# Kernel tuning notes

Measured on AMD Instinct MI355X. Metric: run time of the kernel, lower is better.

Reference implementation:

```python
import jax, jax.numpy as jnp
import numpy as np
from jax import lax

N, G, E0, K = 16384, 128, 262144, 8   # nodes, graphs, initial edges, knn k
NF, D = 3, 8                          # num_features, smallest_dim


def _lin(key, fi, fo):
    k1, k2 = jax.random.split(key)
    lim = 1.0 / np.sqrt(fi)
    return (jax.random.uniform(k1, (fi, fo), minval=-lim, maxval=lim),
            jax.random.uniform(k2, (fo,), minval=-lim, maxval=lim))


def setup_inputs():
    key = jax.random.key(0)
    ks = jax.random.split(key, 16)
    x = jax.random.normal(ks[0], (N, NF), dtype=jnp.float32)
    edge_index = jax.random.randint(ks[1], (2, E0), 0, N, dtype=jnp.int32)
    batch = jnp.repeat(jnp.arange(G, dtype=jnp.int32), N // G)  # sorted graph ids
    p = {}
    dims = [("c1", 2 * NF, 2 * D, 2 * D), ("c2", 4 * D, D, D),
            ("c3", 2 * D, D, D), ("c4", 2 * D, 2 * D, 2 * D)]
    i = 2
    for name, fi, fh, fo in dims:
        p[name + "w1"], p[name + "b1"] = _lin(ks[i], fi, fh); i += 1
        p[name + "w2"], p[name + "b2"] = _lin(ks[i], fh, fo); i += 1
    p["fc3w"], p["fc3b"] = _lin(ks[i], 2 * D, 2 * NF); i += 1
    p["outw"], p["outb"] = _lin(ks[i], 2 * NF, 1)
    return {"x": x, "edge_index": edge_index, "batch": batch, **p}


def _edge_conv(x, src, dst, w1, b1, w2, b2):
    # PyG EdgeConv: message = MLP([x_i, x_j - x_i]), aggr='max' over incoming edges
    xi, xj = x[dst], x[src]
    m = jnp.concatenate([xi, xj - xi], axis=-1)        # [E, 2F]
    m = jax.nn.relu(m @ w1 + b1) @ w2 + b2             # [E, Fout]
    agg = jax.ops.segment_max(m, dst, num_segments=x.shape[0])
    return jnp.where(jnp.isfinite(agg), agg, 0.0)      # nodes w/o edges -> 0


def _knn_edges(x, k):
    # PyG knn_graph (no batch arg, loop=False, flow='source_to_target')
    n = x.shape[0]
    sq = jnp.sum(x * x, axis=1)
    d = sq[:, None] + sq[None, :] - 2.0 * (x @ x.T)    # [N, N] squared dists
    d = d.at[jnp.arange(n), jnp.arange(n)].set(jnp.inf)  # exclude self
    _, idx = lax.top_k(-d, k)                          # [N, k] nearest neighbors
    src = idx.reshape(-1).astype(jnp.int32)            # neighbor -> source
    dst = jnp.repeat(jnp.arange(n, dtype=jnp.int32), k)  # query -> target
    return src, dst


def reference(x, edge_index, batch,
              c1w1, c1b1, c1w2, c1b2, c2w1, c2b1, c2w2, c2b2,
              c3w1, c3b1, c3w2, c3b2, c4w1, c4b1, c4w2, c4b2,
              fc3w, fc3b, outw, outb):
    src0, dst0 = edge_index[0], edge_index[1]
    # encoder
    h = jax.nn.relu(_edge_conv(x, src0, dst0, c1w1, c1b1, c1w2, c1b2))
    h = jax.nn.relu(_edge_conv(h, src0, dst0, c2w1, c2b1, c2w2, c2b2))
    # dynamic graph rebuild
    src, dst = _knn_edges(h, K)
    # decoder (topk=False path: batch = data.batch)
    h = jax.nn.relu(_edge_conv(h, src, dst, c3w1, c3b1, c3w2, c3b2))
    h = jax.nn.relu(_edge_conv(h, src, dst, c4w1, c4b1, c4w2, c4b2))
    g = jax.ops.segment_max(h, batch, num_segments=G)  # global max pool [G, 2D]
    g = jnp.where(jnp.isfinite(g), g, 0.0)
    g = jax.nn.relu(g @ fc3w + fc3b)
    return jax.nn.sigmoid(g @ outw + outb)             # [G, 1]
```

## Files before the change

kernel.cpp:

```cpp
#include <hip/hip_runtime.h>
#include <math.h>

#define NN 16384
#define GG 128
#define KK 8
#define SCAP 96
#define TCAP 14
#define DCAP 64

__device__ __forceinline__ unsigned fkey(float x) {
  unsigned u = __float_as_uint(x);
  return (u & 0x80000000u) ? ~u : (u | 0x80000000u);
}

__device__ __forceinline__ float rdist2(const float* q, float4 c0, float4 c1,
                                        float sc) {
  float acc = fmaf(q[0], c0.x, sc);
  acc = fmaf(q[1], c0.y, acc);
  acc = fmaf(q[2], c0.z, acc);
  acc = fmaf(q[3], c0.w, acc);
  acc = fmaf(q[4], c1.x, acc);
  acc = fmaf(q[5], c1.y, acc);
  acc = fmaf(q[6], c1.z, acc);
  acc = fmaf(q[7], c1.w, acc);
  return acc;
}

__device__ __forceinline__ float4 neg2(float4 v) {
  return make_float4(-2.f * v.x, -2.f * v.y, -2.f * v.z, -2.f * v.w);
}

__global__ void k_build(const int* __restrict__ ei, int E,
                        int* __restrict__ deg, int* __restrict__ eidx) {
  int e = blockIdx.x * 256 + threadIdx.x;
  if (e >= E) return;
  int dv = ei[E + e];
  int slot = atomicAdd(&deg[dv], 1);
  if (slot < DCAP) eidx[dv * DCAP + slot] = e;
}

__global__ __launch_bounds__(256) void k_conv1g(
    const float* __restrict__ x, const int* __restrict__ ei,
    const int* __restrict__ deg, const int* __restrict__ eidx,
    const float* __restrict__ w1, const float* __restrict__ b1,
    const float* __restrict__ w2, const float* __restrict__ b2,
    float* __restrict__ h1out) {
  __shared__ float sw1[96], sb1[16], sw2[256], sb2[16];
  for (int t = threadIdx.x; t < 96; t += 256) sw1[t] = w1[t];
  for (int t = threadIdx.x; t < 256; t += 256) sw2[t] = w2[t];
  if (threadIdx.x < 16) {
    sb1[threadIdx.x] = b1[threadIdx.x];
    sb2[threadIdx.x] = b2[threadIdx.x];
  }
  __syncthreads();
  int tid = blockIdx.x * 256 + threadIdx.x;
  int i = tid >> 3, r = tid & 7;
  float xi0 = x[i * 3 + 0], xi1 = x[i * 3 + 1], xi2 = x[i * 3 + 2];
  float acc[16];
#pragma unroll
  for (int t = 0; t < 16; t++) acc[t] = -INFINITY;
  int n = deg[i];
  n = (n < DCAP) ? n : DCAP;
  for (int k = r; k < n; k += 8) {
    int e = eidx[i * DCAP + k];
    int s = ei[e];
    float m[6] = {xi0,
                  xi1,
                  xi2,
                  x[s * 3 + 0] - xi0,
                  x[s * 3 + 1] - xi1,
                  x[s * 3 + 2] - xi2};
    float hid[16];
#pragma unroll
    for (int o = 0; o < 16; o++) {
      float a = sb1[o];
#pragma unroll
      for (int f = 0; f < 6; f++) a = fmaf(m[f], sw1[f * 16 + o], a);
      hid[o] = fmaxf(a, 0.f);
    }
#pragma unroll
    for (int o = 0; o < 16; o++) {
      float a = sb2[o];
#pragma unroll
      for (int hh = 0; hh < 16; hh++) a = fmaf(hid[hh], sw2[hh * 16 + o], a);
      acc[o] = fmaxf(acc[o], a);
    }
  }
#pragma unroll
  for (int mm = 1; mm < 8; mm <<= 1) {
#pragma unroll
    for (int c = 0; c < 16; c++) acc[c] = fmaxf(acc[c], __shfl_xor(acc[c], mm));
  }
  if (r == 0) {
    float4* op = (float4*)(h1out + (size_t)i * 16);
    op[0] = make_float4(fmaxf(acc[0], 0.f), fmaxf(acc[1], 0.f),
                        fmaxf(acc[2], 0.f), fmaxf(acc[3], 0.f));
    op[1] = make_float4(fmaxf(acc[4], 0.f), fmaxf(acc[5], 0.f),
                        fmaxf(acc[6], 0.f), fmaxf(acc[7], 0.f));
    op[2] = make_float4(fmaxf(acc[8], 0.f), fmaxf(acc[9], 0.f),
                        fmaxf(acc[10], 0.f), fmaxf(acc[11], 0.f));
    op[3] = make_float4(fmaxf(acc[12], 0.f), fmaxf(acc[13], 0.f),
                        fmaxf(acc[14], 0.f), fmaxf(acc[15], 0.f));
  }
}

__global__ __launch_bounds__(256) void k_conv2g(
    const float* __restrict__ h1f, const int* __restrict__ ei,
    const int* __restrict__ deg, const int* __restrict__ eidx,
    const float* __restrict__ w1, const float* __restrict__ b1,
    const float* __restrict__ w2, const float* __restrict__ b2,
    float* __restrict__ h2out, float* __restrict__ sqn) {
  __shared__ float sw1[256], sb1[8], sw2[64], sb2[8];
  for (int t = threadIdx.x; t < 256; t += 256) sw1[t] = w1[t];
  if (threadIdx.x < 64) sw2[threadIdx.x] = w2[threadIdx.x];
  if (threadIdx.x < 8) {
    sb1[threadIdx.x] = b1[threadIdx.x];
    sb2[threadIdx.x] = b2[threadIdx.x];
  }
  __syncthreads();
  int tid = blockIdx.x * 256 + threadIdx.x;
  int i = tid >> 3, r = tid & 7;
  const float4* ip = (const float4*)(h1f + (size_t)i * 16);
  float4 a0 = ip[0], a1 = ip[1], a2 = ip[2], a3 = ip[3];
  float vi[16] = {a0.x, a0.y, a0.z, a0.w, a1.x, a1.y, a1.z, a1.w,
                  a2.x, a2.y, a2.z, a2.w, a3.x, a3.y, a3.z, a3.w};
  float acc[8];
#pragma unroll
  for (int t = 0; t < 8; t++) acc[t] = -INFINITY;
  int n = deg[i];
  n = (n < DCAP) ? n : DCAP;
  for (int k = r; k < n; k += 8) {
    int e = eidx[i * DCAP + k];
    int s = ei[e];
    const float4* jp = (const float4*)(h1f + (size_t)s * 16);
    float4 c0 = jp[0], c1 = jp[1], c2 = jp[2], c3 = jp[3];
    float vj[16] = {c0.x, c0.y, c0.z, c0.w, c1.x, c1.y, c1.z, c1.w,
                    c2.x, c2.y, c2.z, c2.w, c3.x, c3.y, c3.z, c3.w};
    float hid[8];
#pragma unroll
    for (int o = 0; o < 8; o++) {
      float a = sb1[o];
#pragma unroll
      for (int f = 0; f < 16; f++) a = fmaf(vi[f], sw1[f * 8 + o], a);
#pragma unroll
      for (int f = 0; f < 16; f++)
        a = fmaf(vj[f] - vi[f], sw1[(16 + f) * 8 + o], a);
      hid[o] = fmaxf(a, 0.f);
    }
#pragma unroll
    for (int o = 0; o < 8; o++) {
      float a = sb2[o];
#pragma unroll
      for (int hh = 0; hh < 8; hh++) a = fmaf(hid[hh], sw2[hh * 8 + o], a);
      acc[o] = fmaxf(acc[o], a);
    }
  }
#pragma unroll
  for (int mm = 1; mm < 8; mm <<= 1) {
#pragma unroll
    for (int c = 0; c < 8; c++) acc[c] = fmaxf(acc[c], __shfl_xor(acc[c], mm));
  }
  if (r == 0) {
    float v[8];
    float s2 = 0.f;
#pragma unroll
    for (int c = 0; c < 8; c++) {
      v[c] = fmaxf(acc[c], 0.f);
      s2 += v[c] * v[c];
    }
    float4* op = (float4*)(h2out + (size_t)i * 8);
    op[0] = make_float4(v[0], v[1], v[2], v[3]);
    op[1] = make_float4(v[4], v[5], v[6], v[7]);
    sqn[i] = s2;
  }
}

__global__ __launch_bounds__(256) void k_tau_part(
    const float* __restrict__ h2f, const float* __restrict__ sqn,
    float* __restrict__ taupart) {
  __shared__ float sh[512 * 8];
  __shared__ float ss[512];
  int qb = blockIdx.x & 63;
  int scn = blockIdx.x >> 6;
  int i = qb * 256 + threadIdx.x;
  const float4* qp = (const float4*)(h2f + (size_t)i * 8);
  float4 q0 = qp[0], q1 = qp[1];
  float q[8] = {q0.x, q0.y, q0.z, q0.w, q1.x, q1.y, q1.z, q1.w};
  int base = scn * 512;
  for (int cc = threadIdx.x; cc < 512; cc += 256) {
    const float4* src = (const float4*)(h2f + (size_t)(base + cc) * 8);
    ((float4*)sh)[cc * 2] = neg2(src[0]);
    ((float4*)sh)[cc * 2 + 1] = neg2(src[1]);
    ss[cc] = sqn[base + cc];
  }
  __syncthreads();
  float bd[8];
#pragma unroll
  for (int t = 0; t < 8; t++) bd[t] = INFINITY;
  int self = i - base;
#pragma unroll 2
  for (int c = 0; c < 512; c++) {
    const float4* cp = (const float4*)(sh + c * 8);
    float r = rdist2(q, cp[0], cp[1], ss[c]);
    float cd = (c == self) ? INFINITY : r;
#pragma unroll
    for (int t = 0; t < 8; t++) {
      float lo = fminf(cd, bd[t]);
      cd = fmaxf(cd, bd[t]);
      bd[t] = lo;
    }
  }
  float* dst = taupart + ((size_t)scn * NN + i) * 8;
#pragma unroll
  for (int t = 0; t < 8; t++) dst[t] = bd[t];
}

__global__ void k_tau_merge(const float* __restrict__ taupart,
                            float* __restrict__ tau) {
  int i = blockIdx.x * blockDim.x + threadIdx.x;
  if (i >= NN) return;
  float bd[8];
#pragma unroll
  for (int t = 0; t < 8; t++) bd[t] = INFINITY;
  for (int scn = 0; scn < 8; scn++) {
    const float* p = taupart + ((size_t)scn * NN + i) * 8;
#pragma unroll
    for (int c = 0; c < 8; c++) {
      float cd = p[c];
#pragma unroll
      for (int t = 0; t < 8; t++) {
        float lo = fminf(cd, bd[t]);
        cd = fmaxf(cd, bd[t]);
        bd[t] = lo;
      }
    }
  }
  tau[i] = bd[7];
}

__global__ __launch_bounds__(256, 4) void k_knn_collect(
    const float* __restrict__ h2f, const float* __restrict__ sqn,
    const float* __restrict__ tau, int* __restrict__ qcnt,
    unsigned long long* __restrict__ surv) {
  __shared__ float sh[256 * 8];
  __shared__ float ss[256];
  __shared__ unsigned long long pbuf[TCAP * 256];
  int qb = blockIdx.x & 15;
  int ch = blockIdx.x >> 4;
  float q[4][8];
  float thr[4];
#pragma unroll
  for (int s = 0; s < 4; s++) {
    int ii = qb * 1024 + threadIdx.x + s * 256;
    const float4* qp = (const float4*)(h2f + (size_t)ii * 8);
    float4 a = qp[0], b = qp[1];
    q[s][0] = a.x; q[s][1] = a.y; q[s][2] = a.z; q[s][3] = a.w;
    q[s][4] = b.x; q[s][5] = b.y; q[s][6] = b.z; q[s][7] = b.w;
    thr[s] = tau[ii];
  }
  int base = ch * 256;
  {
    const float4* src = (const float4*)(h2f + (size_t)(base + threadIdx.x) * 8);
    ((float4*)sh)[threadIdx.x * 2] = neg2(src[0]);
    ((float4*)sh)[threadIdx.x * 2 + 1] = neg2(src[1]);
    ss[threadIdx.x] = sqn[base + threadIdx.x];
  }
  __syncthreads();
  int cnt = 0;
#pragma unroll 2
  for (int c = 0; c < 256; c++) {
    const float4* cp = (const float4*)(sh + c * 8);
    float4 c0 = cp[0], c1 = cp[1];
    float sc = ss[c];
#pragma unroll
    for (int s = 0; s < 4; s++) {
      float r = rdist2(q[s], c0, c1, sc);
      if (__any(r <= thr[s])) {
        int j = base + c;
        int iqs = qb * 1024 + threadIdx.x + s * 256;
        if (r <= thr[s] && j != iqs) {
          if (cnt < TCAP)
            pbuf[cnt * 256 + threadIdx.x] =
                ((unsigned long long)fkey(r) << 32) | (unsigned)(s << 14) |
                (unsigned)j;
          cnt++;
        }
      }
    }
  }
  int n = (cnt < TCAP) ? cnt : TCAP;
  for (int k = 0; k < n; k++) {
    unsigned long long e = pbuf[k * 256 + threadIdx.x];
    int s = (int)((e >> 14) & 3u);
    unsigned long long key = e & 0xFFFFFFFF00003FFFull;
    int qi = qb * 1024 + threadIdx.x + s * 256;
    int slot = atomicAdd(&qcnt[qi], 1);
    if (slot < SCAP) surv[(size_t)qi * SCAP + slot] = key;
  }
}

__global__ __launch_bounds__(256) void k_mc3(
    const float* __restrict__ h2f, const int* __restrict__ qcnt,
    const unsigned long long* __restrict__ surv,
    const float* __restrict__ w1, const float* __restrict__ b1,
    const float* __restrict__ w2, const float* __restrict__ b2,
    int* __restrict__ kn, float* __restrict__ h3) {
  __shared__ float sw1[128], sb1[8], sw2[64], sb2[8];
  if (threadIdx.x < 128) sw1[threadIdx.x] = w1[threadIdx.x];
  if (threadIdx.x < 64) sw2[threadIdx.x] = w2[threadIdx.x];
  if (threadIdx.x < 8) {
    sb1[threadIdx.x] = b1[threadIdx.x];
    sb2[threadIdx.x] = b2[threadIdx.x];
  }
  __syncthreads();
  int tid = blockIdx.x * 256 + threadIdx.x;
  int i = tid >> 3, r = tid & 7;
  int n = qcnt[i];
  n = (n < SCAP) ? n : SCAP;
  unsigned long long bk[8];
#pragma unroll
  for (int t = 0; t < 8; t++) bk[t] = ~0ull;
  const unsigned long long* p = surv + (size_t)i * SCAP;
  for (int k = 0; k < n; k++) {
    unsigned long long key = p[k];
    if (key < bk[7]) {
#pragma unroll
      for (int t = 0; t < 8; t++) {
        bool lt = key < bk[t];
        unsigned long long lo = lt ? key : bk[t];
        key = lt ? bk[t] : key;
        bk[t] = lo;
      }
    }
  }
  int j = (int)(unsigned)bk[r];
  kn[i * 8 + r] = j;
  const float4* hp = (const float4*)h2f;
  float4 a0 = hp[i * 2 + 0], a1 = hp[i * 2 + 1];
  float4 c0 = hp[j * 2 + 0], c1 = hp[j * 2 + 1];
  float m[16] = {a0.x,        a0.y,        a0.z,        a0.w,
                 a1.x,        a1.y,        a1.z,        a1.w,
                 c0.x - a0.x, c0.y - a0.y, c0.z - a0.z, c0.w - a0.w,
                 c1.x - a1.x, c1.y - a1.y, c1.z - a1.z, c1.w - a1.w};
  float hid[8];
#pragma unroll
  for (int o = 0; o < 8; o++) {
    float a = sb1[o];
#pragma unroll
    for (int f = 0; f < 16; f++) a = fmaf(m[f], sw1[f * 8 + o], a);
    hid[o] = fmaxf(a, 0.f);
  }
  float o8[8];
#pragma unroll
  for (int o = 0; o < 8; o++) {
    float a = sb2[o];
#pragma unroll
    for (int hh = 0; hh < 8; hh++) a = fmaf(hid[hh], sw2[hh * 8 + o], a);
    o8[o] = a;
  }
#pragma unroll
  for (int mm = 1; mm < 8; mm <<= 1) {
#pragma unroll
    for (int c = 0; c < 8; c++) o8[c] = fmaxf(o8[c], __shfl_xor(o8[c], mm));
  }
  if (r == 0) {
    float4* op = (float4*)(h3 + i * 8);
    op[0] = make_float4(fmaxf(o8[0], 0.f), fmaxf(o8[1], 0.f),
                        fmaxf(o8[2], 0.f), fmaxf(o8[3], 0.f));
    op[1] = make_float4(fmaxf(o8[4], 0.f), fmaxf(o8[5], 0.f),
                        fmaxf(o8[6], 0.f), fmaxf(o8[7], 0.f));
  }
}

__global__ __launch_bounds__(1024) void k_conv4pool(
    const float* __restrict__ h3, const int* __restrict__ knn,
    const float* __restrict__ w1, const float* __restrict__ b1,
    const float* __restrict__ w2, const float* __restrict__ b2,
    const float* __restrict__ fc3w, const float* __restrict__ fc3b,
    const float* __restrict__ outw, const float* __restrict__ outb,
    float* __restrict__ out) {
  __shared__ float sw1[256], sb1[16], sw2[256], sb2[16];
  __shared__ float pl[128 * 16];
  __shared__ float gm[16];
  int g = blockIdx.x, tid = threadIdx.x;
  if (tid < 256) {
    sw1[tid] = w1[tid];
    sw2[tid] = w2[tid];
  }
  if (tid < 16) {
    sb1[tid] = b1[tid];
    sb2[tid] = b2[tid];
  }
  __syncthreads();
  int nl = tid >> 3, r = tid & 7;
  int i = g * 128 + nl;
  int j = knn[g * 1024 + tid];
  const float4* hp = (const float4*)h3;
  float4 a0 = hp[i * 2 + 0], a1 = hp[i * 2 + 1];
  float4 c0 = hp[j * 2 + 0], c1 = hp[j * 2 + 1];
  float m[16] = {a0.x,        a0.y,        a0.z,        a0.w,
                 a1.x,        a1.y,        a1.z,        a1.w,
                 c0.x - a0.x, c0.y - a0.y, c0.z - a0.z, c0.w - a0.w,
                 c1.x - a1.x, c1.y - a1.y, c1.z - a1.z, c1.w - a1.w};
  float hid[16];
#pragma unroll
  for (int o = 0; o < 16; o++) {
    float a = sb1[o];
#pragma unroll
    for (int f = 0; f < 16; f++) a = fmaf(m[f], sw1[f * 16 + o], a);
    hid[o] = fmaxf(a, 0.f);
  }
  float o16[16];
#pragma unroll
  for (int o = 0; o < 16; o++) {
    float a = sb2[o];
#pragma unroll
    for (int hh = 0; hh < 16; hh++) a = fmaf(hid[hh], sw2[hh * 16 + o], a);
    o16[o] = a;
  }
#pragma unroll
  for (int mm = 1; mm < 8; mm <<= 1) {
#pragma unroll
    for (int c = 0; c < 16; c++) o16[c] = fmaxf(o16[c], __shfl_xor(o16[c], mm));
  }
  if (r == 0) {
#pragma unroll
    for (int c = 0; c < 16; c++) pl[nl * 16 + c] = fmaxf(o16[c], 0.f);
  }
  __syncthreads();
  if (tid < 16) {
    float v = pl[tid];
    for (int n = 1; n < 128; n++) v = fmaxf(v, pl[n * 16 + tid]);
    gm[tid] = v;
  }
  __syncthreads();
  if (tid == 0) {
    float f3[6];
#pragma unroll
    for (int o = 0; o < 6; o++) {
      float acc = fc3b[o];
#pragma unroll
      for (int cc = 0; cc < 16; cc++)
        acc = fmaf(gm[cc], fc3w[cc * 6 + o], acc);
      f3[o] = fmaxf(acc, 0.f);
    }
    float z = outb[0];
#pragma unroll
    for (int o = 0; o < 6; o++) z = fmaf(f3[o], outw[o], z);
    out[g] = 1.f / (1.f + expf(-z));
  }
}

extern "C" void kernel_launch(void* const* d_in, const int* in_sizes, int n_in,
                              void* d_out, int out_size, void* d_ws,
                              size_t ws_size, hipStream_t stream) {
  const float* x = (const float*)d_in[0];
  const int* ei = (const int*)d_in[1];
  const float* c1w1 = (const float*)d_in[3];
  const float* c1b1 = (const float*)d_in[4];
  const float* c1w2 = (const float*)d_in[5];
  const float* c1b2 = (const float*)d_in[6];
  const float* c2w1 = (const float*)d_in[7];
  const float* c2b1 = (const float*)d_in[8];
  const float* c2w2 = (const float*)d_in[9];
  const float* c2b2 = (const float*)d_in[10];
  const float* c3w1 = (const float*)d_in[11];
  const float* c3b1 = (const float*)d_in[12];
  const float* c3w2 = (const float*)d_in[13];
  const float* c3b2 = (const float*)d_in[14];
  const float* c4w1 = (const float*)d_in[15];
  const float* c4b1 = (const float*)d_in[16];
  const float* c4w2 = (const float*)d_in[17];
  const float* c4b2 = (const float*)d_in[18];
  const float* fc3w = (const float*)d_in[19];
  const float* fc3b = (const float*)d_in[20];
  const float* outw = (const float*)d_in[21];
  const float* outb = (const float*)d_in[22];
  float* out = (float*)d_out;
  int E = in_sizes[1] / 2;

  char* w = (char*)d_ws;
  float* h1f = (float*)w;  w += (size_t)NN * 16 * 4;
  float* h2f = (float*)w;  w += (size_t)NN * 8 * 4;
  float* sqn = (float*)w;  w += (size_t)NN * 4;
  float* tau = (float*)w;  w += (size_t)NN * 4;
  int* kn = (int*)w;       w += (size_t)NN * 8 * 4;
  float* h3 = (float*)w;   w += (size_t)NN * 8 * 4;
  int* deg = (int*)w;      w += (size_t)NN * 4;
  int* qcnt = (int*)w;     w += (size_t)NN * 4;
  w = (char*)(((size_t)w + 255) & ~(size_t)255);
  int* eidx = (int*)w;     w += (size_t)NN * DCAP * 4;
  w = (char*)(((size_t)w + 255) & ~(size_t)255);
  unsigned long long* surv = (unsigned long long*)w;
  float* taupart = (float*)w;

  hipMemsetAsync(deg, 0, (size_t)NN * 2 * 4, stream);
  k_build<<<(E + 255) / 256, 256, 0, stream>>>(ei, E, deg, eidx);
  k_conv1g<<<NN * 8 / 256, 256, 0, stream>>>(x, ei, deg, eidx, c1w1, c1b1,
                                             c1w2, c1b2, h1f);
  k_conv2g<<<NN * 8 / 256, 256, 0, stream>>>(h1f, ei, deg, eidx, c2w1, c2b1,
                                             c2w2, c2b2, h2f, sqn);
  k_tau_part<<<512, 256, 0, stream>>>(h2f, sqn, taupart);
  k_tau_merge<<<NN / 256, 256, 0, stream>>>(taupart, tau);
  k_knn_collect<<<16 * 64, 256, 0, stream>>>(h2f, sqn, tau, qcnt, surv);
  k_mc3<<<NN * 8 / 256, 256, 0, stream>>>(h2f, qcnt, surv, c3w1, c3b1, c3w2,
                                          c3b2, kn, h3);
  k_conv4pool<<<GG, 1024, 0, stream>>>(h3, kn, c4w1, c4b1, c4w2, c4b2, fc3w,
                                       fc3b, outw, outb, out);
}
```

Measured before the change: 260.4 us.

## Replace atomic survivor lists with per-chunk fixed slots and recompute distances

The kNN collect kernel no longer stages packed distance/index keys in shared memory and appends them through per-query atomics. Each block now writes up to 8 16-bit candidate indices per (query, chunk) slot plus a byte count, using smaller chunks of 128 and twice as many blocks. The merge kernel walks all 128 chunk slots per query and recomputes distances from h2f before insertion sorting. This removes the atomics and the shared staging buffer at the cost of redundant distance recomputation, gathered reads in the merge, and a serial 128-iteration count scan per query. It also drops candidates past 8 per chunk, which could lose true neighbours if many fall in one chunk.

```diff
diff --git a/kernel.cpp b/kernel.cpp
--- a/kernel.cpp
+++ b/kernel.cpp
@@ -4,8 +4,9 @@
 #define NN 16384
 #define GG 128
 #define KK 8
-#define SCAP 96
-#define TCAP 14
+#define NCH 128
+#define CHSZ 128
+#define QCAP 8
 #define DCAP 64
 
 __device__ __forceinline__ unsigned fkey(float x) {
@@ -238,37 +239,35 @@
   tau[i] = bd[7];
 }
 
-__global__ __launch_bounds__(256, 4) void k_knn_collect(
+__global__ __launch_bounds__(256, 8) void k_knn_collect(
     const float* __restrict__ h2f, const float* __restrict__ sqn,
-    const float* __restrict__ tau, int* __restrict__ qcnt,
-    unsigned long long* __restrict__ surv) {
-  __shared__ float sh[256 * 8];
-  __shared__ float ss[256];
-  __shared__ unsigned long long pbuf[TCAP * 256];
+    const float* __restrict__ tau, unsigned char* __restrict__ cntT,
+    unsigned short* __restrict__ survT) {
+  __shared__ float sh[CHSZ * 8];
+  __shared__ float ss[CHSZ];
   int qb = blockIdx.x & 15;
   int ch = blockIdx.x >> 4;
   float q[4][8];
   float thr[4];
+  int iq[4];
+  int cnt[4] = {0, 0, 0, 0};
 #pragma unroll
   for (int s = 0; s < 4; s++) {
     int ii = qb * 1024 + threadIdx.x + s * 256;
+    iq[s] = ii;
     const float4* qp = (const float4*)(h2f + (size_t)ii * 8);
     float4 a = qp[0], b = qp[1];
     q[s][0] = a.x; q[s][1] = a.y; q[s][2] = a.z; q[s][3] = a.w;
     q[s][4] = b.x; q[s][5] = b.y; q[s][6] = b.z; q[s][7] = b.w;
     thr[s] = tau[ii];
   }
-  int base = ch * 256;
-  {
-    const float4* src = (const float4*)(h2f + (size_t)(base + threadIdx.x) * 8);
-    ((float4*)sh)[threadIdx.x * 2] = neg2(src[0]);
-    ((float4*)sh)[threadIdx.x * 2 + 1] = neg2(src[1]);
-    ss[threadIdx.x] = sqn[base + threadIdx.x];
-  }
-  __syncthreads();
-  int cnt = 0;
+  int base = ch * CHSZ;
+  ((float4*)sh)[threadIdx.x] =
+      neg2(((const float4*)(h2f + (size_t)base * 8))[threadIdx.x]);
+  if (threadIdx.x < CHSZ) ss[threadIdx.x] = sqn[base + threadIdx.x];
+  __syncthreads();
 #pragma unroll 2
-  for (int c = 0; c < 256; c++) {
+  for (int c = 0; c < CHSZ; c++) {
     const float4* cp = (const float4*)(sh + c * 8);
     float4 c0 = cp[0], c1 = cp[1];
     float sc = ss[c];
@@ -277,31 +276,25 @@
       float r = rdist2(q[s], c0, c1, sc);
       if (__any(r <= thr[s])) {
         int j = base + c;
-        int iqs = qb * 1024 + threadIdx.x + s * 256;
-        if (r <= thr[s] && j != iqs) {
-          if (cnt < TCAP)
-            pbuf[cnt * 256 + threadIdx.x] =
-                ((unsigned long long)fkey(r) << 32) | (unsigned)(s << 14) |
-                (unsigned)j;
-          cnt++;
+        if (r <= thr[s] && j != iq[s]) {
+          if (cnt[s] < QCAP)
+            survT[((size_t)iq[s] * NCH + ch) * QCAP + cnt[s]] =
+                (unsigned short)j;
+          cnt[s]++;
         }
       }
     }
   }
-  int n = (cnt < TCAP) ? cnt : TCAP;
-  for (int k = 0; k < n; k++) {
-    unsigned long long e = pbuf[k * 256 + threadIdx.x];
-    int s = (int)((e >> 14) & 3u);
-    unsigned long long key = e & 0xFFFFFFFF00003FFFull;
-    int qi = qb * 1024 + threadIdx.x + s * 256;
-    int slot = atomicAdd(&qcnt[qi], 1);
-    if (slot < SCAP) surv[(size_t)qi * SCAP + slot] = key;
-  }
+#pragma unroll
+  for (int s = 0; s < 4; s++)
+    cntT[(size_t)iq[s] * NCH + ch] =
+        (unsigned char)(cnt[s] < QCAP ? cnt[s] : QCAP);
 }
 
 __global__ __launch_bounds__(256) void k_mc3(
-    const float* __restrict__ h2f, const int* __restrict__ qcnt,
-    const unsigned long long* __restrict__ surv,
+    const float* __restrict__ h2f, const float* __restrict__ sqn,
+    const unsigned char* __restrict__ cntT,
+    const unsigned short* __restrict__ survT,
     const float* __restrict__ w1, const float* __restrict__ b1,
     const float* __restrict__ w2, const float* __restrict__ b2,
     int* __restrict__ kn, float* __restrict__ h3) {
@@ -315,21 +308,31 @@
   __syncthreads();
   int tid = blockIdx.x * 256 + threadIdx.x;
   int i = tid >> 3, r = tid & 7;
-  int n = qcnt[i];
-  n = (n < SCAP) ? n : SCAP;
+  const float4* qp = (const float4*)(h2f + (size_t)i * 8);
+  float4 qa = qp[0], qb4 = qp[1];
+  float q[8] = {qa.x, qa.y, qa.z, qa.w, qb4.x, qb4.y, qb4.z, qb4.w};
   unsigned long long bk[8];
 #pragma unroll
   for (int t = 0; t < 8; t++) bk[t] = ~0ull;
-  const unsigned long long* p = surv + (size_t)i * SCAP;
-  for (int k = 0; k < n; k++) {
-    unsigned long long key = p[k];
-    if (key < bk[7]) {
-#pragma unroll
-      for (int t = 0; t < 8; t++) {
-        bool lt = key < bk[t];
-        unsigned long long lo = lt ? key : bk[t];
-        key = lt ? bk[t] : key;
-        bk[t] = lo;
+  const unsigned char* crow = cntT + (size_t)i * NCH;
+  const unsigned short* srow = survT + (size_t)i * NCH * QCAP;
+  for (int ch = 0; ch < NCH; ch++) {
+    int c8 = crow[ch];
+    for (int k = 0; k < c8; k++) {
+      int j = srow[ch * QCAP + k];
+      const float4* cp = (const float4*)(h2f + (size_t)j * 8);
+      float4 c0 = neg2(cp[0]), c1 = neg2(cp[1]);
+      float rr = rdist2(q, c0, c1, sqn[j]);
+      unsigned long long key =
+          ((unsigned long long)fkey(rr) << 32) | (unsigned)j;
+      if (key < bk[7]) {
+#pragma unroll
+        for (int t = 0; t < 8; t++) {
+          bool lt = key < bk[t];
+          unsigned long long lo = lt ? key : bk[t];
+          key = lt ? bk[t] : key;
+          bk[t] = lo;
+        }
       }
     }
   }
@@ -487,14 +490,15 @@
   int* kn = (int*)w;       w += (size_t)NN * 8 * 4;
   float* h3 = (float*)w;   w += (size_t)NN * 8 * 4;
   int* deg = (int*)w;      w += (size_t)NN * 4;
-  int* qcnt = (int*)w;     w += (size_t)NN * 4;
   w = (char*)(((size_t)w + 255) & ~(size_t)255);
   int* eidx = (int*)w;     w += (size_t)NN * DCAP * 4;
   w = (char*)(((size_t)w + 255) & ~(size_t)255);
-  unsigned long long* surv = (unsigned long long*)w;
+  unsigned char* cntT = (unsigned char*)w; w += (size_t)NN * NCH;
+  w = (char*)(((size_t)w + 255) & ~(size_t)255);
+  unsigned short* survT = (unsigned short*)w;
   float* taupart = (float*)w;
 
-  hipMemsetAsync(deg, 0, (size_t)NN * 2 * 4, stream);
+  hipMemsetAsync(deg, 0, (size_t)NN * 4, stream);
   k_build<<<(E + 255) / 256, 256, 0, stream>>>(ei, E, deg, eidx);
   k_conv1g<<<NN * 8 / 256, 256, 0, stream>>>(x, ei, deg, eidx, c1w1, c1b1,
                                              c1w2, c1b2, h1f);
@@ -502,9 +506,9 @@
                                              c2w2, c2b2, h2f, sqn);
   k_tau_part<<<512, 256, 0, stream>>>(h2f, sqn, taupart);
   k_tau_merge<<<NN / 256, 256, 0, stream>>>(taupart, tau);
-  k_knn_collect<<<16 * 64, 256, 0, stream>>>(h2f, sqn, tau, qcnt, surv);
-  k_mc3<<<NN * 8 / 256, 256, 0, stream>>>(h2f, qcnt, surv, c3w1, c3b1, c3w2,
-                                          c3b2, kn, h3);
+  k_knn_collect<<<16 * NCH, 256, 0, stream>>>(h2f, sqn, tau, cntT, survT);
+  k_mc3<<<NN * 8 / 256, 256, 0, stream>>>(h2f, sqn, cntT, survT, c3w1, c3b1,
+                                          c3w2, c3b2, kn, h3);
   k_conv4pool<<<GG, 1024, 0, stream>>>(h3, kn, c4w1, c4b1, c4w2, c4b2, fc3w,
                                        fc3b, outw, outb, out);
 }
```

After: 328.3 us. 1.26x slower.
